# Kernel tuning notes

Hardware: AMD Instinct MI355X
Metric: run time of the kernel (lower is better)

The kernel has to match this reference:

```python
import jax, jax.numpy as jnp
import numpy as np

NUM_HEADS = 16
NUM_KV_HEADS = 4
ROPE_THETA = 10000.0


def apply_rope(x, position_ids, theta):
    # x: [B, S, h, d]; position_ids: [B, S]
    d = x.shape[-1]
    freqs = 1.0 / theta ** (jnp.arange(0, d, 2, dtype=jnp.float32) / d)  # [d/2]
    angles = position_ids.astype(jnp.float32)[..., None] * freqs          # [B, S, d/2]
    cos = jnp.cos(angles)[:, :, None, :]                                  # [B, S, 1, d/2]
    sin = jnp.sin(angles)[:, :, None, :]
    xr = x.astype(jnp.float32).reshape(*x.shape[:-1], d // 2, 2)
    x0, x1 = xr[..., 0], xr[..., 1]
    o0 = x0 * cos - x1 * sin
    o1 = x0 * sin + x1 * cos
    out = jnp.stack((o0, o1), axis=-1).reshape(*x.shape)
    return out.astype(x.dtype)


def setup_inputs() -> dict:
    key = jax.random.key(0)
    k0, k1, k2, k3, k4 = jax.random.split(key, 5)
    B, S, H = 1, 2048, 2048
    Hkv = H // (NUM_HEADS // NUM_KV_HEADS)  # 512
    init_scale = 0.02 / np.sqrt(H)
    return {
        "hidden_states": jax.random.normal(k0, (B, S, H), jnp.float32),
        "attention_mask": jnp.ones((B, S), jnp.int32),
        "segment_ids": jnp.zeros((B, S), jnp.int32),
        "position_ids": jnp.broadcast_to(jnp.arange(S, dtype=jnp.int32)[None], (B, S)),
        "Wq": jax.random.normal(k1, (H, H), jnp.float32) * init_scale,
        "Wk": jax.random.normal(k2, (H, Hkv), jnp.float32) * init_scale,
        "Wv": jax.random.normal(k3, (H, Hkv), jnp.float32) * init_scale,
        "Wo": jax.random.normal(k4, (H, H), jnp.float32) * init_scale,
    }


def reference(hidden_states, attention_mask, segment_ids, position_ids, Wq, Wk, Wv, Wo):
    B, S, H = hidden_states.shape
    nh, nkv = NUM_HEADS, NUM_KV_HEADS
    g = nh // nkv
    hd = H // nh

    xq = (hidden_states @ Wq).reshape(B, S, nh, hd)
    xk = (hidden_states @ Wk).reshape(B, S, nkv, hd)
    xv = (hidden_states @ Wv).reshape(B, S, nkv, hd)
    # GQA repeat: 'b s (h d) -> b s (h g) d' == repeat each kv head g times contiguously
    xk = jnp.repeat(xk, g, axis=2)  # [B, S, nh, hd]
    xv = jnp.repeat(xv, g, axis=2)

    xq = apply_rope(xq, position_ids, ROPE_THETA)
    xk = apply_rope(xk, position_ids, ROPE_THETA)

    # masks: causal AND padding AND segment
    causal = jnp.tril(jnp.ones((S, S), dtype=bool))[None, None]            # [1,1,S,S]
    pad = (attention_mask > 0)[:, None, None, :]                            # [B,1,1,S]
    seg = (segment_ids[:, :, None] == segment_ids[:, None, :])[:, None]     # [B,1,S,S]
    mask = causal & pad & seg                                               # [B,1,S,S]

    scale = 1.0 / np.sqrt(hd)
    logits = jnp.einsum("bqhd,bkhd->bhqk", xq.astype(jnp.float32), xk.astype(jnp.float32)) * scale
    logits = jnp.where(mask, logits, jnp.finfo(jnp.float32).min)
    probs = jax.nn.softmax(logits, axis=-1).astype(xv.dtype)
    attn = jnp.einsum("bhqk,bkhd->bqhd", probs, xv)                         # [B,S,nh,hd]

    out = attn.reshape(B, S, H) @ Wo
    return out
```

## Files before the change

kernel.cpp:

```cpp
#include <hip/hip_runtime.h>
#include <hip/hip_bf16.h>
#include <stdint.h>
#include <math.h>

#define SS 2048
#define HH 2048
#define NH 16
#define NKV 4
#define HD 128
#define HKV 512
#define NQKV 3072
#define QPAIRS (HH / 2)
#define KPAIRS (HKV / 2)
#define TPAIRS (QPAIRS + KPAIRS)

typedef __bf16 bf16x8 __attribute__((ext_vector_type(8)));
typedef float f32x4 __attribute__((ext_vector_type(4)));

static_assert(sizeof(bf16x8) == 16, "bf16x8 must be 16B");

__device__ __forceinline__ void async_ld16(const void* gp, void* lp) {
  __builtin_amdgcn_global_load_lds(
      (const __attribute__((address_space(1))) unsigned int*)(uintptr_t)gp,
      (__attribute__((address_space(3))) unsigned int*)(uintptr_t)lp,
      16, 0, 0);
}

__device__ __forceinline__ unsigned short f2bu(float f) {
  __hip_bfloat16 b = __float2bfloat16(f);
  return *reinterpret_cast<unsigned short*>(&b);
}

__global__ void k_cvt(const float4* __restrict__ src, ushort4* __restrict__ dst, int n4) {
  int i = blockIdx.x * 256 + threadIdx.x;
  if (i >= n4) return;
  float4 v = src[i];
  ushort4 o;
  o.x = f2bu(v.x); o.y = f2bu(v.y); o.z = f2bu(v.z); o.w = f2bu(v.w);
  dst[i] = o;
}

__global__ void k_transpose_w(const float* __restrict__ Wq, const float* __restrict__ Wk,
                              const float* __restrict__ Wv, const float* __restrict__ Wo,
                              __hip_bfloat16* __restrict__ WqT, __hip_bfloat16* __restrict__ WkT,
                              __hip_bfloat16* __restrict__ WvT, __hip_bfloat16* __restrict__ WoT) {
  __shared__ float tile[32][33];
  const int z = blockIdx.z;
  const float* src = (z == 0) ? Wq : (z == 1) ? Wo : (z == 2) ? Wk : Wv;
  __hip_bfloat16* dst = (z == 0) ? WqT : (z == 1) ? WoT : (z == 2) ? WkT : WvT;
  const int C = (z < 2) ? HH : HKV;
  int bx = blockIdx.x * 32;
  int by = blockIdx.y * 32;
  if (bx >= C) return;
  int tx = threadIdx.x, ty = threadIdx.y;
#pragma unroll
  for (int i = 0; i < 4; i++)
    tile[ty + i * 8][tx] = src[(size_t)(by + ty + i * 8) * C + bx + tx];
  __syncthreads();
#pragma unroll
  for (int i = 0; i < 4; i++)
    dst[(size_t)(bx + ty + i * 8) * HH + by + tx] = __float2bfloat16(tile[tx][ty + i * 8]);
}

__global__ void k_transpose_bf(const __hip_bfloat16* __restrict__ src, __hip_bfloat16* __restrict__ dst,
                               int R, int C, int sstride) {
  __shared__ __hip_bfloat16 tile[32][33];
  int bx = blockIdx.x * 32;
  int by = blockIdx.y * 32;
  int tx = threadIdx.x, ty = threadIdx.y;
#pragma unroll
  for (int i = 0; i < 4; i++)
    tile[ty + i * 8][tx] = src[(size_t)(by + ty + i * 8) * sstride + bx + tx];
  __syncthreads();
#pragma unroll
  for (int i = 0; i < 4; i++)
    dst[(size_t)(bx + ty + i * 8) * R + by + tx] = tile[tx][ty + i * 8];
}

__device__ __forceinline__ void cstore(float* p, float v) { *p = v; }
__device__ __forceinline__ void cstore(__hip_bfloat16* p, float v) { *p = __float2bfloat16(v); }

template <typename OutT>
__global__ __launch_bounds__(256) void k_gemm_bt(
    const __hip_bfloat16* __restrict__ A, const __hip_bfloat16* __restrict__ B,
    OutT* __restrict__ C, int M, int N, int K, int lda, int ldb, int ldc) {
  __shared__ __align__(16) __hip_bfloat16 sA0[128 * 32];
  __shared__ __align__(16) __hip_bfloat16 sB0[128 * 32];
  __shared__ __align__(16) __hip_bfloat16 sA1[128 * 32];
  __shared__ __align__(16) __hip_bfloat16 sB1[128 * 32];
  const int tid = threadIdx.x;
  const int lane = tid & 63;
  const int wave = tid >> 6;
  const int bm = blockIdx.y * 128;
  const int bn = blockIdx.x * 128;
  const int wm = (wave & 1) * 64;
  const int wn = (wave >> 1) * 64;
  const int am = lane & 15;
  const int ch = lane >> 4;

  f32x4 acc[4][4] = {};

  auto stage = [&](__hip_bfloat16* sA, __hip_bfloat16* sB, int k0) {
#pragma unroll
    for (int q = 0; q < 2; q++) {
      int c = q * 256 + tid;
      int row = c >> 2, kp = c & 3;
      int col = (kp ^ ((row >> 1) & 3)) * 8;
      async_ld16(A + (size_t)(bm + row) * lda + k0 + col, (char*)sA + c * 16);
      async_ld16(B + (size_t)(bn + row) * ldb + k0 + col, (char*)sB + c * 16);
    }
  };
  auto compute = [&](const __hip_bfloat16* sA, const __hip_bfloat16* sB) {
    bf16x8 a[4], b[4];
#pragma unroll
    for (int i = 0; i < 4; i++) {
      int row = wm + i * 16 + am;
      a[i] = *(const bf16x8*)(sA + row * 32 + ((ch ^ ((row >> 1) & 3)) * 8));
    }
#pragma unroll
    for (int j = 0; j < 4; j++) {
      int row = wn + j * 16 + am;
      b[j] = *(const bf16x8*)(sB + row * 32 + ((ch ^ ((row >> 1) & 3)) * 8));
    }
#pragma unroll
    for (int i = 0; i < 4; i++)
#pragma unroll
      for (int j = 0; j < 4; j++)
        acc[i][j] = __builtin_amdgcn_mfma_f32_16x16x32_bf16(a[i], b[j], acc[i][j], 0, 0, 0);
  };

  stage(sA0, sB0, 0);
  int k0 = 0;
  while (true) {
    __syncthreads();
    if (k0 + 32 < K) stage(sA1, sB1, k0 + 32);
    compute(sA0, sB0);
    k0 += 32; if (k0 >= K) break;
    __syncthreads();
    if (k0 + 32 < K) stage(sA0, sB0, k0 + 32);
    compute(sA1, sB1);
    k0 += 32; if (k0 >= K) break;
  }

#pragma unroll
  for (int i = 0; i < 4; i++)
#pragma unroll
    for (int j = 0; j < 4; j++)
#pragma unroll
      for (int r = 0; r < 4; r++) {
        int row = bm + wm + i * 16 + ch * 4 + r;
        int col = bn + wn + j * 16 + am;
        cstore(C + (size_t)row * ldc + col, acc[i][j][r]);
      }
}

template <typename OutT>
__global__ __launch_bounds__(256) void k_gemm_bt64(
    const __hip_bfloat16* __restrict__ A, const __hip_bfloat16* __restrict__ B,
    OutT* __restrict__ C, int M, int N, int K, int lda, int ldb, int ldc) {
  __shared__ __align__(16) __hip_bfloat16 sA0[64 * 32];
  __shared__ __align__(16) __hip_bfloat16 sB0[128 * 32];
  __shared__ __align__(16) __hip_bfloat16 sA1[64 * 32];
  __shared__ __align__(16) __hip_bfloat16 sB1[128 * 32];
  const int tid = threadIdx.x;
  const int lane = tid & 63;
  const int wave = tid >> 6;
  const int bm = blockIdx.y * 64;
  const int bn = blockIdx.x * 128;
  const int wm = (wave & 1) * 32;
  const int wn = (wave >> 1) * 64;
  const int am = lane & 15;
  const int ch = lane >> 4;

  f32x4 acc[2][4] = {};

  auto stage = [&](__hip_bfloat16* sA, __hip_bfloat16* sB, int k0) {
    {
      int c = tid;
      int row = c >> 2, kp = c & 3;
      int col = (kp ^ ((row >> 1) & 3)) * 8;
      async_ld16(A + (size_t)(bm + row) * lda + k0 + col, (char*)sA + c * 16);
    }
#pragma unroll
    for (int q = 0; q < 2; q++) {
      int c = q * 256 + tid;
      int row = c >> 2, kp = c & 3;
      int col = (kp ^ ((row >> 1) & 3)) * 8;
      async_ld16(B + (size_t)(bn + row) * ldb + k0 + col, (char*)sB + c * 16);
    }
  };
  auto compute = [&](const __hip_bfloat16* sA, const __hip_bfloat16* sB) {
    bf16x8 a[2], b[4];
#pragma unroll
    for (int i = 0; i < 2; i++) {
      int row = wm + i * 16 + am;
      a[i] = *(const bf16x8*)(sA + row * 32 + ((ch ^ ((row >> 1) & 3)) * 8));
    }
#pragma unroll
    for (int j = 0; j < 4; j++) {
      int row = wn + j * 16 + am;
      b[j] = *(const bf16x8*)(sB + row * 32 + ((ch ^ ((row >> 1) & 3)) * 8));
    }
#pragma unroll
    for (int i = 0; i < 2; i++)
#pragma unroll
      for (int j = 0; j < 4; j++)
        acc[i][j] = __builtin_amdgcn_mfma_f32_16x16x32_bf16(a[i], b[j], acc[i][j], 0, 0, 0);
  };

  stage(sA0, sB0, 0);
  int k0 = 0;
  while (true) {
    __syncthreads();
    if (k0 + 32 < K) stage(sA1, sB1, k0 + 32);
    compute(sA0, sB0);
    k0 += 32; if (k0 >= K) break;
    __syncthreads();
    if (k0 + 32 < K) stage(sA0, sB0, k0 + 32);
    compute(sA1, sB1);
    k0 += 32; if (k0 >= K) break;
  }

#pragma unroll
  for (int i = 0; i < 2; i++)
#pragma unroll
    for (int j = 0; j < 4; j++)
#pragma unroll
      for (int r = 0; r < 4; r++) {
        int row = bm + wm + i * 16 + ch * 4 + r;
        int col = bn + wn + j * 16 + am;
        cstore(C + (size_t)row * ldc + col, acc[i][j][r]);
      }
}

__global__ void k_rope2(const __hip_bfloat16* __restrict__ QKVb,
                        __hip_bfloat16* __restrict__ Qb, __hip_bfloat16* __restrict__ Kb,
                        const int* __restrict__ pos) {
  const float SCL = 0.08838834764831845f * 1.4426950408889634f;
  __shared__ float sFreq[64];
  if (threadIdx.x < 64)
    sFreq[threadIdx.x] = (float)(1.0 / pow(10000.0, (double)threadIdx.x / 64.0));
  __syncthreads();
  int idx = blockIdx.x * 256 + threadIdx.x;
  if (idx >= SS * TPAIRS) return;
  int s = idx / TPAIRS;
  int p = idx - s * TPAIRS;
  bool isq = p < QPAIRS;
  int pp = isq ? p : p - QPAIRS;
  float ang = (float)pos[s] * sFreq[pp & 63];
  float sn, cs;
  sincosf(ang, &sn, &cs);
  const ushort2 v = *(const ushort2*)(QKVb + (size_t)s * NQKV + (isq ? 2 * pp : HH + 2 * pp));
  float x0 = __bfloat162float(*(const __hip_bfloat16*)&v.x);
  float x1 = __bfloat162float(*(const __hip_bfloat16*)&v.y);
  float o0 = x0 * cs - x1 * sn;
  float o1 = x0 * sn + x1 * cs;
  float m = isq ? SCL : 1.0f;
  ushort2 o; o.x = f2bu(o0 * m); o.y = f2bu(o1 * m);
  __hip_bfloat16* dst = isq ? (Qb + (size_t)s * HH + 2 * pp) : (Kb + (size_t)s * HKV + 2 * pp);
  *(ushort2*)dst = o;
}

__global__ __launch_bounds__(256, 2) void k_attn(
    const __hip_bfloat16* __restrict__ Qb,
    const __hip_bfloat16* __restrict__ Kb,
    const __hip_bfloat16* __restrict__ Vt,
    const int* __restrict__ amv, const int* __restrict__ seg,
    __hip_bfloat16* __restrict__ O) {
  __shared__ __align__(16) __hip_bfloat16 sK[2][64 * 128];
  __shared__ __align__(16) __hip_bfloat16 sV[2][128 * 64];
  __shared__ __align__(16) __hip_bfloat16 sPall[4][16 * 64];
  __shared__ int sInfo[2][64];

  const int id = blockIdx.x;
  const int a0 = id & 255;
  const int h = a0 >> 4;
  const int qh = a0 & 15;
  const int qt = (id >> 8) ? (31 - qh) : qh;
  const int kvh = h >> 2;
  const int tid = threadIdx.x, lane = tid & 63, w = tid >> 6;
  const int am = lane & 15, ch = lane >> 4;
  const int qrow0 = qt * 64 + w * 16;
  char* sP = (char*)&sPall[w][0];

  bf16x8 qf[4];
#pragma unroll
  for (int ks = 0; ks < 4; ks++)
    qf[ks] = *(const bf16x8*)(Qb + (size_t)(qrow0 + am) * HH + h * HD + ks * 32 + ch * 8);

  int segq[4];
#pragma unroll
  for (int r = 0; r < 4; r++) segq[r] = seg[qrow0 + ch * 4 + r];

  f32x4 o_acc[8] = {};
  float l_s[4] = {0.f, 0.f, 0.f, 0.f};

  auto stage = [&](int kt, int p) {
#pragma unroll
    for (int q = 0; q < 4; q++) {
      int c = q * 256 + tid;
      int row = c >> 4, kp = c & 15;
      int col = (kp ^ (row & 15)) * 8;
      async_ld16(Kb + (size_t)(kt * 64 + row) * HKV + kvh * 128 + col, (char*)sK[p] + c * 16);
    }
#pragma unroll
    for (int q = 0; q < 4; q++) {
      int c = q * 256 + tid;
      int row = c >> 3, kp = c & 7;
      int col = (kp ^ (row & 7)) * 8;
      async_ld16(Vt + (size_t)(kvh * 128 + row) * SS + kt * 64 + col, (char*)sV[p] + c * 16);
    }
    if (tid < 64) {
      int kidx = kt * 64 + tid;
      sInfo[p][tid] = (amv[kidx] > 0) ? seg[kidx] : 0x7fffffff;
    }
  };

  stage(0, 0);
  for (int kt = 0; kt <= qt; kt++) {
    const int p = kt & 1;
    __syncthreads();
    if (kt < qt) stage(kt + 1, p ^ 1);

    f32x4 sacc[4] = {};
#pragma unroll
    for (int ks = 0; ks < 4; ks++)
#pragma unroll
      for (int jt = 0; jt < 4; jt++) {
        bf16x8 kf = *(const bf16x8*)(sK[p] + (jt * 16 + am) * 128 + (((ks * 4 + ch) ^ am) * 8));
        sacc[jt] = __builtin_amdgcn_mfma_f32_16x16x32_bf16(qf[ks], kf, sacc[jt], 0, 0, 0);
      }

#pragma unroll
    for (int jt = 0; jt < 4; jt++) {
      int kloc = jt * 16 + am;
      int kinfo = sInfo[p][kloc];
#pragma unroll
      for (int r = 0; r < 4; r++) {
        int qrow = qrow0 + ch * 4 + r;
        bool ok = (kinfo == segq[r]) && (kt * 64 + kloc <= qrow);
        float pv = ok ? exp2f(sacc[jt][r] - 8.0f) : 0.0f;
        l_s[r] += pv;
        int row = ch * 4 + r;
        int chunk = (jt * 2 + (am >> 3)) ^ (row & 7);
        *(__hip_bfloat16*)(sP + row * 128 + chunk * 16 + (am & 7) * 2) = __float2bfloat16(pv);
      }
    }

#pragma unroll
    for (int ks = 0; ks < 2; ks++) {
      bf16x8 pf = *(const bf16x8*)(sP + am * 128 + (((ks * 4 + ch) ^ (am & 7)) * 16));
#pragma unroll
      for (int jt = 0; jt < 8; jt++) {
        int vrow = jt * 16 + am;
        bf16x8 vf = *(const bf16x8*)(sV[p] + vrow * 64 + (((ks * 4 + ch) ^ (vrow & 7)) * 8));
        o_acc[jt] = __builtin_amdgcn_mfma_f32_16x16x32_bf16(pf, vf, o_acc[jt], 0, 0, 0);
      }
    }
  }

#pragma unroll
  for (int off = 1; off < 16; off <<= 1)
#pragma unroll
    for (int r = 0; r < 4; r++) l_s[r] += __shfl_xor(l_s[r], off, 64);
  float inv[4];
#pragma unroll
  for (int r = 0; r < 4; r++) inv[r] = 1.0f / l_s[r];
#pragma unroll
  for (int jt = 0; jt < 8; jt++)
#pragma unroll
    for (int r = 0; r < 4; r++) {
      int row = qrow0 + ch * 4 + r;
      O[(size_t)row * HH + h * HD + jt * 16 + am] = __float2bfloat16(o_acc[jt][r] * inv[r]);
    }
}

extern "C" void kernel_launch(void* const* d_in, const int* in_sizes, int n_in,
                              void* d_out, int out_size, void* d_ws, size_t ws_size,
                              hipStream_t stream) {
  const float* X  = (const float*)d_in[0];
  const int* amv  = (const int*)d_in[1];
  const int* seg  = (const int*)d_in[2];
  const int* pos  = (const int*)d_in[3];
  const float* Wq = (const float*)d_in[4];
  const float* Wk = (const float*)d_in[5];
  const float* Wv = (const float*)d_in[6];
  const float* Wo = (const float*)d_in[7];
  float* out = (float*)d_out;

  char* ws = (char*)d_ws;
  size_t off = 0;
  auto alloc = [&](size_t bytes) { void* p = ws + off; off += (bytes + 255) & ~(size_t)255; return p; };
  __hip_bfloat16* Xb   = (__hip_bfloat16*)alloc((size_t)SS * HH * 2);
  __hip_bfloat16* WqT  = (__hip_bfloat16*)alloc((size_t)HH * HH * 2);
  __hip_bfloat16* WkT  = (__hip_bfloat16*)alloc((size_t)HKV * HH * 2);
  __hip_bfloat16* WvT  = (__hip_bfloat16*)alloc((size_t)HKV * HH * 2);
  __hip_bfloat16* WoT  = (__hip_bfloat16*)alloc((size_t)HH * HH * 2);
  __hip_bfloat16* QKVb = (__hip_bfloat16*)alloc((size_t)SS * NQKV * 2);
  __hip_bfloat16* Qb   = (__hip_bfloat16*)alloc((size_t)SS * HH * 2);
  __hip_bfloat16* Kb   = (__hip_bfloat16*)alloc((size_t)SS * HKV * 2);
  __hip_bfloat16* Vt   = (__hip_bfloat16*)alloc((size_t)HKV * SS * 2);
  __hip_bfloat16* Ab   = (__hip_bfloat16*)alloc((size_t)SS * HH * 2);
  (void)WkT; (void)WvT;

  k_cvt<<<(SS * HH / 4 + 255) / 256, 256, 0, stream>>>((const float4*)X, (ushort4*)Xb, SS * HH / 4);
  k_transpose_w<<<dim3(64, 64, 4), dim3(32, 8), 0, stream>>>(Wq, Wk, Wv, Wo, WqT, WkT, WvT, WoT);
  k_gemm_bt64<__hip_bfloat16><<<dim3(NQKV / 128, SS / 64), 256, 0, stream>>>(
      Xb, WqT, QKVb, SS, NQKV, HH, HH, HH, NQKV);
  k_rope2<<<(SS * TPAIRS + 255) / 256, 256, 0, stream>>>(QKVb, Qb, Kb, pos);
  k_transpose_bf<<<dim3(HKV / 32, SS / 32), dim3(32, 8), 0, stream>>>(QKVb + HH + HKV, Vt, SS, HKV, NQKV);
  k_attn<<<dim3(512), 256, 0, stream>>>(Qb, Kb, Vt, amv, seg, Ab);
  k_gemm_bt<float><<<dim3(HH / 128, SS / 128), 256, 0, stream>>>(Ab, WoT, out, SS, HH, HH, HH, HH, HH);
}
```

Measured before the change: 267.5 us.

## Merge prep kernels, shrink attention KV tile, use 64-row GEMM for output

Merges the X conversion and weight transposes into one launch, and the RoPE and V transpose into another, to cut launch overhead. The attention kernel now uses 32-key tiles instead of 64, with half the shared memory and launch bounds raised to 4 blocks per CU, to improve occupancy. The output projection switches to the 64-row GEMM variant for more blocks. Together these touch several unrelated parts and trade per-tile work for more synchronisation in attention.

```diff
diff --git a/kernel.cpp b/kernel.cpp
--- a/kernel.cpp
+++ b/kernel.cpp
@@ -31,27 +31,31 @@
   return *reinterpret_cast<unsigned short*>(&b);
 }
 
-__global__ void k_cvt(const float4* __restrict__ src, ushort4* __restrict__ dst, int n4) {
-  int i = blockIdx.x * 256 + threadIdx.x;
-  if (i >= n4) return;
-  float4 v = src[i];
-  ushort4 o;
-  o.x = f2bu(v.x); o.y = f2bu(v.y); o.z = f2bu(v.z); o.w = f2bu(v.w);
-  dst[i] = o;
-}
-
-__global__ void k_transpose_w(const float* __restrict__ Wq, const float* __restrict__ Wk,
-                              const float* __restrict__ Wv, const float* __restrict__ Wo,
-                              __hip_bfloat16* __restrict__ WqT, __hip_bfloat16* __restrict__ WkT,
-                              __hip_bfloat16* __restrict__ WvT, __hip_bfloat16* __restrict__ WoT) {
+__global__ __launch_bounds__(256) void k_prep1(
+    const float* __restrict__ X, const float* __restrict__ Wq, const float* __restrict__ Wk,
+    const float* __restrict__ Wv, const float* __restrict__ Wo,
+    __hip_bfloat16* __restrict__ Xb, __hip_bfloat16* __restrict__ WqT,
+    __hip_bfloat16* __restrict__ WkT, __hip_bfloat16* __restrict__ WvT,
+    __hip_bfloat16* __restrict__ WoT) {
   __shared__ float tile[32][33];
-  const int z = blockIdx.z;
-  const float* src = (z == 0) ? Wq : (z == 1) ? Wo : (z == 2) ? Wk : Wv;
-  __hip_bfloat16* dst = (z == 0) ? WqT : (z == 1) ? WoT : (z == 2) ? WkT : WvT;
-  const int C = (z < 2) ? HH : HKV;
-  int bx = blockIdx.x * 32;
-  int by = blockIdx.y * 32;
-  if (bx >= C) return;
+  int b = blockIdx.x;
+  if (b < 4096) {
+    int i = b * 256 + threadIdx.y * 32 + threadIdx.x;
+    float4 v = ((const float4*)X)[i];
+    ushort4 o;
+    o.x = f2bu(v.x); o.y = f2bu(v.y); o.z = f2bu(v.z); o.w = f2bu(v.w);
+    ((ushort4*)Xb)[i] = o;
+    return;
+  }
+  b -= 4096;
+  const float* src; __hip_bfloat16* dst; int xtiles;
+  if (b < 4096)      { src = Wq; dst = WqT; xtiles = 64; }
+  else if (b < 8192) { src = Wo; dst = WoT; xtiles = 64; b -= 4096; }
+  else if (b < 9216) { src = Wk; dst = WkT; xtiles = 16; b -= 8192; }
+  else               { src = Wv; dst = WvT; xtiles = 16; b -= 9216; }
+  const int C = xtiles * 32;
+  int bx = (b % xtiles) * 32;
+  int by = (b / xtiles) * 32;
   int tx = threadIdx.x, ty = threadIdx.y;
 #pragma unroll
   for (int i = 0; i < 4; i++)
@@ -62,100 +66,57 @@
     dst[(size_t)(bx + ty + i * 8) * HH + by + tx] = __float2bfloat16(tile[tx][ty + i * 8]);
 }
 
-__global__ void k_transpose_bf(const __hip_bfloat16* __restrict__ src, __hip_bfloat16* __restrict__ dst,
-                               int R, int C, int sstride) {
-  __shared__ __hip_bfloat16 tile[32][33];
-  int bx = blockIdx.x * 32;
-  int by = blockIdx.y * 32;
+__global__ __launch_bounds__(256) void k_prep2(
+    const __hip_bfloat16* __restrict__ QKVb, __hip_bfloat16* __restrict__ Qb,
+    __hip_bfloat16* __restrict__ Kb, __hip_bfloat16* __restrict__ Vt,
+    const int* __restrict__ pos) {
+  __shared__ float sFreq[64];
+  __shared__ __hip_bfloat16 btile[32][33];
+  int b = blockIdx.x;
+  int tid = threadIdx.y * 32 + threadIdx.x;
+  if (b < 10240) {
+    const float SCL = 0.08838834764831845f * 1.4426950408889634f;
+    if (tid < 64)
+      sFreq[tid] = (float)(1.0 / pow(10000.0, (double)tid / 64.0));
+    __syncthreads();
+    int idx = b * 256 + tid;
+    int s = idx / TPAIRS;
+    int p = idx - s * TPAIRS;
+    bool isq = p < QPAIRS;
+    int pp = isq ? p : p - QPAIRS;
+    float ang = (float)pos[s] * sFreq[pp & 63];
+    float sn, cs;
+    sincosf(ang, &sn, &cs);
+    const ushort2 v = *(const ushort2*)(QKVb + (size_t)s * NQKV + (isq ? 2 * pp : HH + 2 * pp));
+    float x0 = __bfloat162float(*(const __hip_bfloat16*)&v.x);
+    float x1 = __bfloat162float(*(const __hip_bfloat16*)&v.y);
+    float o0 = x0 * cs - x1 * sn;
+    float o1 = x0 * sn + x1 * cs;
+    float m = isq ? SCL : 1.0f;
+    ushort2 o; o.x = f2bu(o0 * m); o.y = f2bu(o1 * m);
+    __hip_bfloat16* dst = isq ? (Qb + (size_t)s * HH + 2 * pp) : (Kb + (size_t)s * HKV + 2 * pp);
+    *(ushort2*)dst = o;
+    return;
+  }
+  b -= 10240;
+  const __hip_bfloat16* src = QKVb + HH + HKV;
+  int bx = (b & 15) * 32;
+  int by = (b >> 4) * 32;
   int tx = threadIdx.x, ty = threadIdx.y;
 #pragma unroll
   for (int i = 0; i < 4; i++)
-    tile[ty + i * 8][tx] = src[(size_t)(by + ty + i * 8) * sstride + bx + tx];
+    btile[ty + i * 8][tx] = src[(size_t)(by + ty + i * 8) * NQKV + bx + tx];
   __syncthreads();
 #pragma unroll
   for (int i = 0; i < 4; i++)
-    dst[(size_t)(bx + ty + i * 8) * R + by + tx] = tile[tx][ty + i * 8];
+    Vt[(size_t)(bx + ty + i * 8) * SS + by + tx] = btile[tx][ty + i * 8];
 }
 
 __device__ __forceinline__ void cstore(float* p, float v) { *p = v; }
 __device__ __forceinline__ void cstore(__hip_bfloat16* p, float v) { *p = __float2bfloat16(v); }
 
 template <typename OutT>
-__global__ __launch_bounds__(256) void k_gemm_bt(
-    const __hip_bfloat16* __restrict__ A, const __hip_bfloat16* __restrict__ B,
-    OutT* __restrict__ C, int M, int N, int K, int lda, int ldb, int ldc) {
-  __shared__ __align__(16) __hip_bfloat16 sA0[128 * 32];
-  __shared__ __align__(16) __hip_bfloat16 sB0[128 * 32];
-  __shared__ __align__(16) __hip_bfloat16 sA1[128 * 32];
-  __shared__ __align__(16) __hip_bfloat16 sB1[128 * 32];
-  const int tid = threadIdx.x;
-  const int lane = tid & 63;
-  const int wave = tid >> 6;
-  const int bm = blockIdx.y * 128;
-  const int bn = blockIdx.x * 128;
-  const int wm = (wave & 1) * 64;
-  const int wn = (wave >> 1) * 64;
-  const int am = lane & 15;
-  const int ch = lane >> 4;
-
-  f32x4 acc[4][4] = {};
-
-  auto stage = [&](__hip_bfloat16* sA, __hip_bfloat16* sB, int k0) {
-#pragma unroll
-    for (int q = 0; q < 2; q++) {
-      int c = q * 256 + tid;
-      int row = c >> 2, kp = c & 3;
-      int col = (kp ^ ((row >> 1) & 3)) * 8;
-      async_ld16(A + (size_t)(bm + row) * lda + k0 + col, (char*)sA + c * 16);
-      async_ld16(B + (size_t)(bn + row) * ldb + k0 + col, (char*)sB + c * 16);
-    }
-  };
-  auto compute = [&](const __hip_bfloat16* sA, const __hip_bfloat16* sB) {
-    bf16x8 a[4], b[4];
-#pragma unroll
-    for (int i = 0; i < 4; i++) {
-      int row = wm + i * 16 + am;
-      a[i] = *(const bf16x8*)(sA + row * 32 + ((ch ^ ((row >> 1) & 3)) * 8));
-    }
-#pragma unroll
-    for (int j = 0; j < 4; j++) {
-      int row = wn + j * 16 + am;
-      b[j] = *(const bf16x8*)(sB + row * 32 + ((ch ^ ((row >> 1) & 3)) * 8));
-    }
-#pragma unroll
-    for (int i = 0; i < 4; i++)
-#pragma unroll
-      for (int j = 0; j < 4; j++)
-        acc[i][j] = __builtin_amdgcn_mfma_f32_16x16x32_bf16(a[i], b[j], acc[i][j], 0, 0, 0);
-  };
-
-  stage(sA0, sB0, 0);
-  int k0 = 0;
-  while (true) {
-    __syncthreads();
-    if (k0 + 32 < K) stage(sA1, sB1, k0 + 32);
-    compute(sA0, sB0);
-    k0 += 32; if (k0 >= K) break;
-    __syncthreads();
-    if (k0 + 32 < K) stage(sA0, sB0, k0 + 32);
-    compute(sA1, sB1);
-    k0 += 32; if (k0 >= K) break;
-  }
-
-#pragma unroll
-  for (int i = 0; i < 4; i++)
-#pragma unroll
-    for (int j = 0; j < 4; j++)
-#pragma unroll
-      for (int r = 0; r < 4; r++) {
-        int row = bm + wm + i * 16 + ch * 4 + r;
-        int col = bn + wn + j * 16 + am;
-        cstore(C + (size_t)row * ldc + col, acc[i][j][r]);
-      }
-}
-
-template <typename OutT>
-__global__ __launch_bounds__(256) void k_gemm_bt64(
+__global__ __launch_bounds__(256, 4) void k_gemm_bt64(
     const __hip_bfloat16* __restrict__ A, const __hip_bfloat16* __restrict__ B,
     OutT* __restrict__ C, int M, int N, int K, int lda, int ldb, int ldc) {
   __shared__ __align__(16) __hip_bfloat16 sA0[64 * 32];
@@ -233,44 +194,16 @@
       }
 }
 
-__global__ void k_rope2(const __hip_bfloat16* __restrict__ QKVb,
-                        __hip_bfloat16* __restrict__ Qb, __hip_bfloat16* __restrict__ Kb,
-                        const int* __restrict__ pos) {
-  const float SCL = 0.08838834764831845f * 1.4426950408889634f;
-  __shared__ float sFreq[64];
-  if (threadIdx.x < 64)
-    sFreq[threadIdx.x] = (float)(1.0 / pow(10000.0, (double)threadIdx.x / 64.0));
-  __syncthreads();
-  int idx = blockIdx.x * 256 + threadIdx.x;
-  if (idx >= SS * TPAIRS) return;
-  int s = idx / TPAIRS;
-  int p = idx - s * TPAIRS;
-  bool isq = p < QPAIRS;
-  int pp = isq ? p : p - QPAIRS;
-  float ang = (float)pos[s] * sFreq[pp & 63];
-  float sn, cs;
-  sincosf(ang, &sn, &cs);
-  const ushort2 v = *(const ushort2*)(QKVb + (size_t)s * NQKV + (isq ? 2 * pp : HH + 2 * pp));
-  float x0 = __bfloat162float(*(const __hip_bfloat16*)&v.x);
-  float x1 = __bfloat162float(*(const __hip_bfloat16*)&v.y);
-  float o0 = x0 * cs - x1 * sn;
-  float o1 = x0 * sn + x1 * cs;
-  float m = isq ? SCL : 1.0f;
-  ushort2 o; o.x = f2bu(o0 * m); o.y = f2bu(o1 * m);
-  __hip_bfloat16* dst = isq ? (Qb + (size_t)s * HH + 2 * pp) : (Kb + (size_t)s * HKV + 2 * pp);
-  *(ushort2*)dst = o;
-}
-
-__global__ __launch_bounds__(256, 2) void k_attn(
+__global__ __launch_bounds__(256, 4) void k_attn(
     const __hip_bfloat16* __restrict__ Qb,
     const __hip_bfloat16* __restrict__ Kb,
     const __hip_bfloat16* __restrict__ Vt,
     const int* __restrict__ amv, const int* __restrict__ seg,
     __hip_bfloat16* __restrict__ O) {
-  __shared__ __align__(16) __hip_bfloat16 sK[2][64 * 128];
-  __shared__ __align__(16) __hip_bfloat16 sV[2][128 * 64];
-  __shared__ __align__(16) __hip_bfloat16 sPall[4][16 * 64];
-  __shared__ int sInfo[2][64];
+  __shared__ __align__(16) __hip_bfloat16 sK[2][32 * 128];
+  __shared__ __align__(16) __hip_bfloat16 sV[2][128 * 32];
+  __shared__ __align__(16) __hip_bfloat16 sPall[4][16 * 32];
+  __shared__ int sInfo[2][32];
 
   const int id = blockIdx.x;
   const int a0 = id & 255;
@@ -297,66 +230,66 @@
 
   auto stage = [&](int kt, int p) {
 #pragma unroll
-    for (int q = 0; q < 4; q++) {
+    for (int q = 0; q < 2; q++) {
       int c = q * 256 + tid;
       int row = c >> 4, kp = c & 15;
       int col = (kp ^ (row & 15)) * 8;
-      async_ld16(Kb + (size_t)(kt * 64 + row) * HKV + kvh * 128 + col, (char*)sK[p] + c * 16);
-    }
-#pragma unroll
-    for (int q = 0; q < 4; q++) {
+      async_ld16(Kb + (size_t)(kt * 32 + row) * HKV + kvh * 128 + col, (char*)sK[p] + c * 16);
+    }
+#pragma unroll
+    for (int q = 0; q < 2; q++) {
       int c = q * 256 + tid;
-      int row = c >> 3, kp = c & 7;
-      int col = (kp ^ (row & 7)) * 8;
-      async_ld16(Vt + (size_t)(kvh * 128 + row) * SS + kt * 64 + col, (char*)sV[p] + c * 16);
-    }
-    if (tid < 64) {
-      int kidx = kt * 64 + tid;
+      int row = c >> 2, kp = c & 3;
+      int col = (kp ^ (row & 3)) * 8;
+      async_ld16(Vt + (size_t)(kvh * 128 + row) * SS + kt * 32 + col, (char*)sV[p] + c * 16);
+    }
+    if (tid < 32) {
+      int kidx = kt * 32 + tid;
       sInfo[p][tid] = (amv[kidx] > 0) ? seg[kidx] : 0x7fffffff;
     }
   };
 
-  stage(0, 0);
-  for (int kt = 0; kt <= qt; kt++) {
-    const int p = kt & 1;
-    __syncthreads();
-    if (kt < qt) stage(kt + 1, p ^ 1);
-
-    f32x4 sacc[4] = {};
+  auto process = [&](int kt, int p) {
+    f32x4 sacc[2] = {};
 #pragma unroll
     for (int ks = 0; ks < 4; ks++)
 #pragma unroll
-      for (int jt = 0; jt < 4; jt++) {
+      for (int jt = 0; jt < 2; jt++) {
         bf16x8 kf = *(const bf16x8*)(sK[p] + (jt * 16 + am) * 128 + (((ks * 4 + ch) ^ am) * 8));
         sacc[jt] = __builtin_amdgcn_mfma_f32_16x16x32_bf16(qf[ks], kf, sacc[jt], 0, 0, 0);
       }
-
-#pragma unroll
-    for (int jt = 0; jt < 4; jt++) {
+#pragma unroll
+    for (int jt = 0; jt < 2; jt++) {
       int kloc = jt * 16 + am;
       int kinfo = sInfo[p][kloc];
 #pragma unroll
       for (int r = 0; r < 4; r++) {
         int qrow = qrow0 + ch * 4 + r;
-        bool ok = (kinfo == segq[r]) && (kt * 64 + kloc <= qrow);
+        bool ok = (kinfo == segq[r]) && (kt * 32 + kloc <= qrow);
         float pv = ok ? exp2f(sacc[jt][r] - 8.0f) : 0.0f;
         l_s[r] += pv;
-        int row = ch * 4 + r;
-        int chunk = (jt * 2 + (am >> 3)) ^ (row & 7);
-        *(__hip_bfloat16*)(sP + row * 128 + chunk * 16 + (am & 7) * 2) = __float2bfloat16(pv);
+        int phys = (jt * 2 + (am >> 3)) ^ r;
+        *(__hip_bfloat16*)(sP + (ch * 4 + r) * 64 + phys * 16 + (am & 7) * 2) =
+            __float2bfloat16(pv);
       }
     }
-
-#pragma unroll
-    for (int ks = 0; ks < 2; ks++) {
-      bf16x8 pf = *(const bf16x8*)(sP + am * 128 + (((ks * 4 + ch) ^ (am & 7)) * 16));
-#pragma unroll
-      for (int jt = 0; jt < 8; jt++) {
-        int vrow = jt * 16 + am;
-        bf16x8 vf = *(const bf16x8*)(sV[p] + vrow * 64 + (((ks * 4 + ch) ^ (vrow & 7)) * 8));
-        o_acc[jt] = __builtin_amdgcn_mfma_f32_16x16x32_bf16(pf, vf, o_acc[jt], 0, 0, 0);
-      }
-    }
+    bf16x8 pf = *(const bf16x8*)(sP + am * 64 + ((ch ^ (am & 3)) * 16));
+#pragma unroll
+    for (int jt = 0; jt < 8; jt++) {
+      bf16x8 vf = *(const bf16x8*)(sV[p] + (jt * 16 + am) * 32 + (((ch ^ (am & 3))) * 8));
+      o_acc[jt] = __builtin_amdgcn_mfma_f32_16x16x32_bf16(pf, vf, o_acc[jt], 0, 0, 0);
+    }
+  };
+
+  const int nt = 2 * qt + 2;
+  stage(0, 0);
+  for (int kt = 0; kt < nt; kt += 2) {
+    __syncthreads();
+    stage(kt + 1, 1);
+    process(kt, 0);
+    __syncthreads();
+    if (kt + 2 < nt) stage(kt + 2, 0);
+    process(kt + 1, 1);
   }
 
 #pragma unroll
@@ -403,12 +336,11 @@
   __hip_bfloat16* Ab   = (__hip_bfloat16*)alloc((size_t)SS * HH * 2);
   (void)WkT; (void)WvT;
 
-  k_cvt<<<(SS * HH / 4 + 255) / 256, 256, 0, stream>>>((const float4*)X, (ushort4*)Xb, SS * HH / 4);
-  k_transpose_w<<<dim3(64, 64, 4), dim3(32, 8), 0, stream>>>(Wq, Wk, Wv, Wo, WqT, WkT, WvT, WoT);
+  k_prep1<<<dim3(14336), dim3(32, 8), 0, stream>>>(X, Wq, Wk, Wv, Wo, Xb, WqT, WkT, WvT, WoT);
   k_gemm_bt64<__hip_bfloat16><<<dim3(NQKV / 128, SS / 64), 256, 0, stream>>>(
       Xb, WqT, QKVb, SS, NQKV, HH, HH, HH, NQKV);
-  k_rope2<<<(SS * TPAIRS + 255) / 256, 256, 0, stream>>>(QKVb, Qb, Kb, pos);
-  k_transpose_bf<<<dim3(HKV / 32, SS / 32), dim3(32, 8), 0, stream>>>(QKVb + HH + HKV, Vt, SS, HKV, NQKV);
+  k_prep2<<<dim3(11264), dim3(32, 8), 0, stream>>>(QKVb, Qb, Kb, Vt, pos);
   k_attn<<<dim3(512), 256, 0, stream>>>(Qb, Kb, Vt, amv, seg, Ab);
-  k_gemm_bt<float><<<dim3(HH / 128, SS / 128), 256, 0, stream>>>(Ab, WoT, out, SS, HH, HH, HH, HH, HH);
-}
+  k_gemm_bt64<float><<<dim3(HH / 128, SS / 64), 256, 0, stream>>>(
+      Ab, WoT, out, SS, HH, HH, HH, HH, HH);
+}
```

Result: slower. 286.5 us (+7.1%).
